# Optimization experiments

Hardware: AMD Instinct MI355X
Metric: run time of the kernel (lower is better)

Reference implementation:

```python
import jax, jax.numpy as jnp
import numpy as np

N = 128          # n_nodes (hardcoded groups=128 in the torch module)
TIME_DIM = 16
XYZ_DIM = 63
SIGMA = 0.3
EPS = 0.01
relu = jax.nn.relu


def gconv(x, W, b):
    # grouped 1x1 Conv1d with groups=N: per-node GEMM
    # x: (N, Cin, L), W: (N, Cout, Cin), b: (N, Cout) -> (N, Cout, L)
    return jnp.einsum('ncl,nkc->nkl', x, W) + b[:, :, None]


def setup_inputs() -> dict:
    key = jax.random.key(0)
    ks = iter(jax.random.split(key, 64))

    def W(shape, fan_in):
        return jax.random.normal(next(ks), shape, jnp.float32) / np.float32(np.sqrt(fan_in))

    def bvec(shape):
        return 0.01 * jax.random.normal(next(ks), shape, jnp.float32)

    B, V = 1, 2048
    inp = {
        'poses': 0.1 * jax.random.normal(next(ks), (B, N, 24, 3), jnp.float32),
        't_ped': jax.random.normal(next(ks), (B, TIME_DIM), jnp.float32),
        'w': jax.random.uniform(next(ks), (N, 24), jnp.float32),
        'wpts': jax.random.uniform(next(ks), (B, V, 3), jnp.float32),
        'nodes_posed': jax.random.uniform(next(ks), (B, N, 3), jnp.float32),
        'local_coords': jax.random.normal(next(ks), (N, B, V, XYZ_DIM), jnp.float32),
        # encoder grouped convs
        'Wec1': W((N, 64, 72 + TIME_DIM), 72 + TIME_DIM), 'bec1': bvec((N, 64)),
        'Wec21': W((N, 8, 64), 64), 'bec21': bvec((N, 8)),
        'Wec22': W((N, 8, 64), 64), 'bec22': bvec((N, 8)),
        # decoder grouped convs
        'Wdc1': W((N, 64, 80), 80), 'bdc1': bvec((N, 64)),
        'Wdc21': W((N, 32, 64), 64), 'bdc21': bvec((N, 32)),
        'Wdc22': W((N, 3, 64), 64), 'bdc22': bvec((N, 3)),
        # feature-field grouped convs
        'Wf1': W((N, 64, 32 + XYZ_DIM), 32 + XYZ_DIM), 'bf1': bvec((N, 64)),
        'Wf2': W((N, 64, 64), 64), 'bf2': bvec((N, 64)),
        'Wf3': W((N, 64, 64), 64), 'bf3': bvec((N, 64)),
        'Wf4': W((N, 256, 64), 64), 'bf4': bvec((N, 256)),
        # Nerf head linears
        'Wc1': W((256, 64), 256), 'bc1': bvec((64,)),
        'Wc2': W((64, 3), 64), 'bc2': bvec((3,)),
        'Wd1': W((256, 1), 256), 'bd1': bvec((1,)),
    }
    return inp


def reference(poses, t_ped, w, wpts, nodes_posed, local_coords,
              Wec1, bec1, Wec21, bec21, Wec22, bec22,
              Wdc1, bdc1, Wdc21, bdc21, Wdc22, bdc22,
              Wf1, bf1, Wf2, bf2, Wf3, bf3, Wf4, bf4,
              Wc1, bc1, Wc2, bc2, Wd1, bd1):
    B, V = poses.shape[0], wpts.shape[1]

    # attention-weighted poses: (B, N, 72)
    poses_w = (w[None, :, :, None] * poses).reshape(B, N, 72)

    # ---- encode ----
    t = jnp.broadcast_to(t_ped[:, None, :], (B, N, TIME_DIM))
    enc_in = jnp.concatenate([poses_w, t], axis=-1).transpose(1, 2, 0)   # (N, 72+td, B)
    net = relu(gconv(enc_in, Wec1, bec1))                                # (N, 64, B)
    mean = gconv(net, Wec21, bec21).transpose(0, 2, 1)                   # (N, B, 8)
    logvar = gconv(net, Wec22, bec22).transpose(0, 2, 1)                 # (N, B, 8)
    z = mean  # eval-mode reparameterize

    # ---- decode ----
    dec_in = jnp.concatenate([poses_w, z.transpose(1, 0, 2)], axis=-1).transpose(1, 2, 0)  # (N, 80, B)
    net = relu(gconv(dec_in, Wdc1, bdc1))
    ei = gconv(net, Wdc21, bdc21).transpose(0, 2, 1)                     # (N, B, 32)
    delta_ni = gconv(net, Wdc22, bdc22).transpose(0, 2, 1)               # (N, B, 3)

    # ---- blend weights: RBF influence of each node on each point ----
    diff = wpts[None, :, :, :] - nodes_posed.transpose(1, 0, 2)[:, :, None, :]  # (N, B, V, 3)
    d2 = jnp.sum(diff * diff, axis=-1)                                   # (N, B, V)
    influ = jnp.exp(-d2 / (2.0 * SIGMA * SIGMA)) - EPS
    mask = influ >= 0
    bweights = jnp.maximum(influ, 0.0)

    # ---- feature field (dense per-node MLP, masked; == padded gather/scatter) ----
    raw = jnp.concatenate([jnp.broadcast_to(ei[:, :, None, :], (N, B, V, 32)),
                           local_coords], axis=-1)                       # (N, B, V, 32+xyz)
    x = raw.reshape(N, B * V, 32 + XYZ_DIM).transpose(0, 2, 1)           # (N, Cin, B*V)
    net = relu(gconv(x, Wf1, bf1))
    net = relu(gconv(net, Wf2, bf2))
    net = relu(gconv(net, Wf3, bf3))
    fout = relu(gconv(net, Wf4, bf4))                                    # (N, 256, B*V)
    f = fout.transpose(0, 2, 1).reshape(N, B, V, 256) * mask[..., None].astype(fout.dtype)

    # ---- blend features ----
    bw = bweights.transpose(1, 2, 0) + 1e-7                              # (B, V, N)
    bw = bw / jnp.sum(bw, axis=-1, keepdims=True)
    f_blend = jnp.einsum('nbvc,bvn->bvc', f, bw)                         # (B, V, 256)

    # ---- Nerf head ----
    netc = relu(f_blend @ Wc1 + bc1)
    c = netc @ Wc2 + bc2                                                 # (B, V, 3)
    d = relu(f_blend @ Wd1 + bd1)                                        # (B, V, 1)
    return (c, d, ei, delta_ni, mean, logvar)
```

## Files before the change

### kernel.cpp

```cpp
#include <hip/hip_runtime.h>

typedef __bf16 bf16;
typedef __bf16 bf16x4 __attribute__((ext_vector_type(4)));
typedef float  f32x4  __attribute__((ext_vector_type(4)));
typedef unsigned short u16x4 __attribute__((ext_vector_type(4)));

#define NPTS 2048
#define LD 68

__global__ __launch_bounds__(256) void k_sniff(const void* poses_raw, int* flag)
{
    __shared__ int cnt;
    if (threadIdx.x == 0) cnt = 0;
    __syncthreads();
    const bf16* pb = (const bf16*)poses_raw;
    int local = 0;
    for (int i = threadIdx.x; i < 9216; i += 256) {
        float v = (float)pb[i];
        if (!(v >= -2.0f && v <= 2.0f)) local++;
    }
    atomicAdd(&cnt, local);
    __syncthreads();
    if (threadIdx.x == 0) *flag = (cnt < 64) ? 1 : 0;
}

template<typename T, int WANT>
__global__ __launch_bounds__(128) void k_encdec_t(
    const T* __restrict__ poses, const T* __restrict__ t_ped, const T* __restrict__ w,
    const T* __restrict__ Wec1, const T* __restrict__ bec1,
    const T* __restrict__ Wec21, const T* __restrict__ bec21,
    const T* __restrict__ Wec22, const T* __restrict__ bec22,
    const T* __restrict__ Wdc1, const T* __restrict__ bdc1,
    const T* __restrict__ Wdc21, const T* __restrict__ bdc21,
    const T* __restrict__ Wdc22, const T* __restrict__ bdc22,
    T* __restrict__ out_ei, T* __restrict__ out_delta,
    T* __restrict__ out_mean, T* __restrict__ out_logvar,
    const int* __restrict__ flag)
{
    if (*flag != WANT) return;
    int n = blockIdx.x, tid = threadIdx.x;
    __shared__ float sin_[88], zbuf[8], net1[64], din[80], net2[64];
    if (tid < 72)      sin_[tid] = (float)w[n*24 + tid/3] * (float)poses[n*72 + tid];
    else if (tid < 88) sin_[tid] = (float)t_ped[tid - 72];
    __syncthreads();
    if (tid < 64) {
        float a = (float)bec1[n*64 + tid];
        const T* wr = Wec1 + (size_t)(n*64 + tid) * 88;
        for (int c = 0; c < 88; ++c) a += (float)wr[c] * sin_[c];
        net1[tid] = fmaxf(a, 0.f);
    }
    __syncthreads();
    if (tid < 8) {
        float a = (float)bec21[n*8 + tid];
        const T* wr = Wec21 + (size_t)(n*8 + tid) * 64;
        for (int c = 0; c < 64; ++c) a += (float)wr[c] * net1[c];
        out_mean[n*8 + tid] = (T)a;
        zbuf[tid] = a;
    } else if (tid < 16) {
        int o = tid - 8;
        float a = (float)bec22[n*8 + o];
        const T* wr = Wec22 + (size_t)(n*8 + o) * 64;
        for (int c = 0; c < 64; ++c) a += (float)wr[c] * net1[c];
        out_logvar[n*8 + o] = (T)a;
    }
    __syncthreads();
    if (tid < 72)      din[tid] = sin_[tid];
    else if (tid < 80) din[tid] = zbuf[tid - 72];
    __syncthreads();
    if (tid < 64) {
        float a = (float)bdc1[n*64 + tid];
        const T* wr = Wdc1 + (size_t)(n*64 + tid) * 80;
        for (int c = 0; c < 80; ++c) a += (float)wr[c] * din[c];
        net2[tid] = fmaxf(a, 0.f);
    }
    __syncthreads();
    if (tid < 32) {
        float a = (float)bdc21[n*32 + tid];
        const T* wr = Wdc21 + (size_t)(n*32 + tid) * 64;
        for (int c = 0; c < 64; ++c) a += (float)wr[c] * net2[c];
        out_ei[n*32 + tid] = (T)a;
    } else if (tid < 35) {
        int o = tid - 32;
        float a = (float)bdc22[n*3 + o];
        const T* wr = Wdc22 + (size_t)(n*3 + o) * 64;
        for (int c = 0; c < 64; ++c) a += (float)wr[c] * net2[c];
        out_delta[n*3 + o] = (T)a;
    }
}

template<typename T, int WANT>
__global__ __launch_bounds__(256) void k_bweights_t(
    const T* __restrict__ wpts, const T* __restrict__ nodes,
    float* __restrict__ wgt, const int* __restrict__ flag)
{
    if (*flag != WANT) return;
    int v = blockIdx.x * 256 + threadIdx.x;
    float px = (float)wpts[v*3+0], py = (float)wpts[v*3+1], pz = (float)wpts[v*3+2];
    float denom = 0.f;
    for (int n = 0; n < 128; ++n) {
        float dx = px - (float)nodes[n*3+0];
        float dy = py - (float)nodes[n*3+1];
        float dz = pz - (float)nodes[n*3+2];
        float d2 = dx*dx + dy*dy + dz*dz;
        float influ = expf(-d2 * (1.0f/0.18f)) - 0.01f;
        denom += fmaxf(influ, 0.f) + 1e-7f;
    }
    float inv = 1.f / denom;
    for (int n = 0; n < 128; ++n) {
        float dx = px - (float)nodes[n*3+0];
        float dy = py - (float)nodes[n*3+1];
        float dz = pz - (float)nodes[n*3+2];
        float d2 = dx*dx + dy*dy + dz*dz;
        float influ = expf(-d2 * (1.0f/0.18f)) - 0.01f;
        wgt[n*NPTS + v] = (influ >= 0.f) ? (fmaxf(influ, 0.f) + 1e-7f) * inv : 0.f;
    }
}

__device__ __forceinline__ f32x4 ld4(const float* p) { return *(const f32x4*)p; }
__device__ __forceinline__ f32x4 ld4(const bf16* p)
{
    bf16x4 v = *(const bf16x4*)p;
    f32x4 r;
    #pragma unroll
    for (int j = 0; j < 4; ++j) r[j] = (float)v[j];
    return r;
}
__device__ __forceinline__ f32x4 ld4_nt(const float* p)
{
    return __builtin_nontemporal_load((const f32x4*)p);
}
__device__ __forceinline__ f32x4 ld4_nt(const bf16* p)
{
    u16x4 u = __builtin_nontemporal_load((const u16x4*)p);
    f32x4 r;
    #pragma unroll
    for (int j = 0; j < 4; ++j) {
        unsigned int bits = ((unsigned int)u[j]) << 16;
        r[j] = __uint_as_float(bits);
    }
    return r;
}

template<typename T, int WANT>
__global__ __launch_bounds__(256) void k_w1prep(
    const T* __restrict__ Wf1, float* __restrict__ W1p, const int* __restrict__ flag)
{
    if (*flag != WANT) return;
    int n = blockIdx.x, tid = threadIdx.x;
    for (int e = tid; e < 6144; e += 256) {
        int oc = e / 96, k = e - oc*96;
        float v = (k < 95) ? (float)Wf1[(size_t)n*6080 + oc*95 + k] : 0.f;
        W1p[(size_t)n*6144 + e] = v;
    }
}

template<typename T>
__device__ __forceinline__ void layer64g(
    const T* __restrict__ W, const T* __restrict__ b,
    const float* __restrict__ hin, float* __restrict__ hout, int og, int pg)
{
    f32x4 acc[4] = {};
    #pragma unroll 4
    for (int k0 = 0; k0 < 64; k0 += 4) {
        f32x4 wv[4], xv[4];
        #pragma unroll
        for (int c = 0; c < 4; ++c) wv[c] = ld4(W + (size_t)(og*4 + c)*64 + k0);
        #pragma unroll
        for (int j = 0; j < 4; ++j) xv[j] = *(const f32x4*)&hin[(k0 + j)*LD + pg*4];
        #pragma unroll
        for (int c = 0; c < 4; ++c)
            #pragma unroll
            for (int j = 0; j < 4; ++j)
                acc[c] += xv[j] * wv[c][j];
    }
    #pragma unroll
    for (int c = 0; c < 4; ++c) {
        float bb = (float)b[og*4 + c];
        f32x4 hv;
        #pragma unroll
        for (int r = 0; r < 4; ++r) hv[r] = fmaxf(acc[c][r] + bb, 0.f);
        *(f32x4*)&hout[(og*4 + c)*LD + pg*4] = hv;
    }
}

template<typename T, int WANT, int W1P>
__global__ __launch_bounds__(256, 3) void k_feat_fast(
    const T* __restrict__ Wf1, const T* __restrict__ Wf2,
    const T* __restrict__ Wf3, const T* __restrict__ Wf4,
    const T* __restrict__ lc, const T* __restrict__ ei,
    const T* __restrict__ bf1, const T* __restrict__ bf2,
    const T* __restrict__ bf3, const T* __restrict__ bf4,
    const float* __restrict__ wgt, const float* __restrict__ W1p,
    int nslice, float* __restrict__ slices, float* __restrict__ f_blend,
    const int* __restrict__ flag)
{
    if (*flag != WANT) return;
    int bid = blockIdx.x;
    int xcd = bid & 7;
    int i   = bid >> 3;
    int g     = 2*xcd + (i >> 5);
    int ptile = i & 31;
    int p0  = ptile * 64;
    int tid = threadIdx.x;
    int og = tid >> 4;
    int pg = tid & 15;

    __shared__ __attribute__((aligned(16))) float smem[(96 + 64) * LD];
    float* xs = smem;
    float* hA = smem + 96*LD;

    if (tid < 64) xs[95*LD + tid] = 0.f;

    f32x4 fb[4][4];
    #pragma unroll
    for (int a = 0; a < 4; ++a)
        #pragma unroll
        for (int c = 0; c < 4; ++c) fb[a][c] = (f32x4){0.f,0.f,0.f,0.f};

    f32x4 lv[4];

    auto stage_load = [&](int n) {
        const T* src = lc + ((size_t)n*NPTS + p0) * 63;
        if (tid < 252) {
            #pragma unroll
            for (int j = 0; j < 4; ++j) lv[j] = ld4_nt(src + tid*16 + j*4);
        }
    };
    auto stage_write = [&](int n) {
        if (tid < 252) {
            #pragma unroll
            for (int j = 0; j < 4; ++j)
                #pragma unroll
                for (int l = 0; l < 4; ++l) {
                    int e = tid*16 + j*4 + l;
                    int p = e/63, c = e - 63*p;
                    xs[(32 + c)*LD + p] = lv[j][l];
                }
        }
        const T* ein = ei + n*32;
        #pragma unroll
        for (int k = 0; k < 8; ++k) {
            int e = k*256 + tid;
            int row = e >> 6, p = e & 63;
            xs[row*LD + p] = (float)ein[row];
        }
    };

    stage_load(g*8);
    stage_write(g*8);
    __syncthreads();

    #pragma unroll 1
    for (int nn = 0; nn < 8; ++nn) {
        int n = g*8 + nn;

        if (W1P) {
            const float* W1b = W1p + (size_t)(n*64 + og*4) * 96;
            f32x4 acc[4] = {};
            #pragma unroll 4
            for (int k0 = 0; k0 < 96; k0 += 4) {
                f32x4 wv[4], xv[4];
                #pragma unroll
                for (int c = 0; c < 4; ++c) wv[c] = ld4(W1b + (size_t)c*96 + k0);
                #pragma unroll
                for (int j = 0; j < 4; ++j) xv[j] = *(const f32x4*)&xs[(k0 + j)*LD + pg*4];
                #pragma unroll
                for (int c = 0; c < 4; ++c)
                    #pragma unroll
                    for (int j = 0; j < 4; ++j)
                        acc[c] += xv[j] * wv[c][j];
            }
            #pragma unroll
            for (int c = 0; c < 4; ++c) {
                float bb = (float)bf1[n*64 + og*4 + c];
                f32x4 hv;
                #pragma unroll
                for (int r = 0; r < 4; ++r) hv[r] = fmaxf(acc[c][r] + bb, 0.f);
                *(f32x4*)&hA[(og*4 + c)*LD + pg*4] = hv;
            }
        } else {
            const T* W1b = Wf1 + (size_t)(n*64 + og*4) * 95;
            f32x4 acc[4] = {};
            #pragma unroll 4
            for (int kk = 0; kk < 23; ++kk) {
                int k0 = kk*4;
                float wv[4][4]; f32x4 xv[4];
                #pragma unroll
                for (int c = 0; c < 4; ++c) {
                    const T* wr = W1b + (size_t)c*95 + k0;
                    #pragma unroll
                    for (int j = 0; j < 4; ++j) wv[c][j] = (float)wr[j];
                }
                #pragma unroll
                for (int j = 0; j < 4; ++j) xv[j] = *(const f32x4*)&xs[(k0 + j)*LD + pg*4];
                #pragma unroll
                for (int c = 0; c < 4; ++c)
                    #pragma unroll
                    for (int j = 0; j < 4; ++j)
                        acc[c] += xv[j] * wv[c][j];
            }
            {
                f32x4 xt[3];
                #pragma unroll
                for (int j = 0; j < 3; ++j) xt[j] = *(const f32x4*)&xs[(92 + j)*LD + pg*4];
                #pragma unroll
                for (int c = 0; c < 4; ++c) {
                    const T* wr = W1b + (size_t)c*95;
                    #pragma unroll
                    for (int j = 0; j < 3; ++j)
                        acc[c] += xt[j] * (float)wr[92 + j];
                }
            }
            #pragma unroll
            for (int c = 0; c < 4; ++c) {
                float bb = (float)bf1[n*64 + og*4 + c];
                f32x4 hv;
                #pragma unroll
                for (int r = 0; r < 4; ++r) hv[r] = fmaxf(acc[c][r] + bb, 0.f);
                *(f32x4*)&hA[(og*4 + c)*LD + pg*4] = hv;
            }
        }
        __syncthreads();

        layer64g(Wf2 + (size_t)n*64*64, bf2 + n*64, hA, xs, og, pg);
        __syncthreads();

        layer64g(Wf3 + (size_t)n*64*64, bf3 + n*64, xs, hA, og, pg);
        __syncthreads();

        if (nn < 7) stage_load(n + 1);

        {
            f32x4 wgtv = ld4_nt(wgt + (size_t)n*NPTS + p0 + pg*4);
            const T* W4n = Wf4 + (size_t)n*256*64;
            const T* b4n = bf4 + n*256;
            #pragma unroll 1
            for (int mt = 0; mt < 4; ++mt) {
                f32x4 acc[4] = {};
                #pragma unroll 4
                for (int k0 = 0; k0 < 64; k0 += 4) {
                    f32x4 wv[4], xv[4];
                    #pragma unroll
                    for (int c = 0; c < 4; ++c)
                        wv[c] = ld4(W4n + (size_t)(mt*64 + og*4 + c)*64 + k0);
                    #pragma unroll
                    for (int j = 0; j < 4; ++j) xv[j] = *(const f32x4*)&hA[(k0 + j)*LD + pg*4];
                    #pragma unroll
                    for (int c = 0; c < 4; ++c)
                        #pragma unroll
                        for (int j = 0; j < 4; ++j)
                            acc[c] += xv[j] * wv[c][j];
                }
                #pragma unroll
                for (int c = 0; c < 4; ++c) {
                    float bb = (float)b4n[mt*64 + og*4 + c];
                    #pragma unroll
                    for (int r = 0; r < 4; ++r)
                        fb[mt][c][r] += fmaxf(acc[c][r] + bb, 0.f) * wgtv[r];
                }
            }
        }
        if (nn < 7) stage_write(n + 1);
        __syncthreads();
    }

    bool atom = (g >= nslice);
    float* dst = atom ? f_blend : (slices + (size_t)g*NPTS*256);
    float* tbuf = smem;
    #pragma unroll 1
    for (int qq = 0; qq < 4; ++qq) {
        if (qq) __syncthreads();
        if ((pg >> 2) == qq) {
            #pragma unroll
            for (int mt = 0; mt < 4; ++mt)
                #pragma unroll
                for (int r = 0; r < 4; ++r) {
                    int row = (pg & 3)*4 + r;
                    f32x4 v = { fb[mt][0][r], fb[mt][1][r], fb[mt][2][r], fb[mt][3][r] };
                    *(f32x4*)&tbuf[row*260 + mt*64 + og*4] = v;
                }
        }
        __syncthreads();
        #pragma unroll
        for (int k = 0; k < 4; ++k) {
            int idx = k*1024 + tid*4;
            int row = idx >> 8, col = idx & 255;
            f32x4 v = *(const f32x4*)&tbuf[row*260 + col];
            size_t o = ((size_t)(p0 + qq*16 + row))*256 + col;
            if (atom) {
                #pragma unroll
                for (int j = 0; j < 4; ++j) atomicAdd(&f_blend[o + j], v[j]);
            } else {
                __builtin_nontemporal_store(v, (f32x4*)&dst[o]);
            }
        }
    }
}

template<int WANT>
__global__ __launch_bounds__(256) void k_reduce(
    const float* __restrict__ slices, float* __restrict__ fbl,
    int nslice, const int* __restrict__ flag)
{
    if (*flag != WANT) return;
    size_t t = (size_t)(blockIdx.x*256 + threadIdx.x) * 4;
    f32x4 s = *(const f32x4*)&fbl[t];
    for (int gg = 0; gg < nslice; ++gg)
        s += __builtin_nontemporal_load((const f32x4*)&slices[(size_t)gg*NPTS*256 + t]);
    *(f32x4*)&fbl[t] = s;
}

__global__ __launch_bounds__(256) void k_zero_fb(float* __restrict__ fb)
{
    fb[blockIdx.x*256 + threadIdx.x] = 0.f;
}

template<typename T, int WANT>
__global__ __launch_bounds__(256) void k_head_t(
    const float* __restrict__ f_blend,
    const T* __restrict__ Wc1, const T* __restrict__ bc1,
    const T* __restrict__ Wc2, const T* __restrict__ bc2,
    const T* __restrict__ Wd1, const T* __restrict__ bd1,
    T* __restrict__ out_c, T* __restrict__ out_d,
    const int* __restrict__ flag)
{
    if (*flag != WANT) return;
    int t = blockIdx.x * 256 + threadIdx.x;
    int p = t >> 6, j = t & 63;
    const float* fb = f_blend + (size_t)p * 256;

    float a = (float)bc1[j];
    #pragma unroll 8
    for (int c = 0; c < 256; ++c)
        a += fb[c] * (float)Wc1[c*64 + j];
    float nc = fmaxf(a, 0.f);

    float s0 = nc * (float)Wc2[j*3 + 0];
    float s1 = nc * (float)Wc2[j*3 + 1];
    float s2 = nc * (float)Wc2[j*3 + 2];
    float sd = 0.f;
    #pragma unroll
    for (int u = 0; u < 4; ++u) {
        int c = j*4 + u;
        sd += fb[c] * (float)Wd1[c];
    }
    #pragma unroll
    for (int off = 32; off > 0; off >>= 1) {
        s0 += __shfl_down(s0, off);
        s1 += __shfl_down(s1, off);
        s2 += __shfl_down(s2, off);
        sd += __shfl_down(sd, off);
    }
    if (j == 0) {
        out_c[p*3 + 0] = (T)(s0 + (float)bc2[0]);
        out_c[p*3 + 1] = (T)(s1 + (float)bc2[1]);
        out_c[p*3 + 2] = (T)(s2 + (float)bc2[2]);
        out_d[p]       = (T)fmaxf(sd + (float)bd1[0], 0.f);
    }
}

extern "C" void kernel_launch(void* const* d_in, const int* in_sizes, int n_in,
                              void* d_out, int out_size, void* d_ws, size_t ws_size,
                              hipStream_t stream)
{
    const size_t SLICE_BYTES = (size_t)NPTS * 256 * 4;
    const size_t W1P_BYTES   = (size_t)128 * 64 * 96 * 4;

    char* wsp = (char*)d_ws;
    auto alloc = [&](size_t bytes) { char* r = wsp; wsp += (bytes + 255) & ~(size_t)255; return r; };
    float* f_blend = (float*)alloc(SLICE_BYTES);
    float* wgt     = (float*)alloc((size_t)128 * NPTS * 4);
    int*   flag    = (int*)  alloc(256);

    float* W1p = nullptr;
    bool use_w1p = ((size_t)(wsp - (char*)d_ws) + W1P_BYTES) <= ws_size;
    if (use_w1p) W1p = (float*)alloc(W1P_BYTES);

    int nslice = 0;
    float* slices = (float*)wsp;
    while (nslice < 16 && ((size_t)(wsp - (char*)d_ws) + SLICE_BYTES) <= ws_size) {
        alloc(SLICE_BYTES);
        nslice++;
    }

    hipLaunchKernelGGL(k_sniff, dim3(1), dim3(256), 0, stream, d_in[0], flag);
    hipLaunchKernelGGL(k_zero_fb, dim3(2048), dim3(256), 0, stream, f_blend);

    #define LAUNCH_ALL(T, WANT)                                                         \
    {                                                                                   \
        const T* poses = (const T*)d_in[0];                                             \
        const T* t_ped = (const T*)d_in[1];                                             \
        const T* w     = (const T*)d_in[2];                                             \
        const T* wpts  = (const T*)d_in[3];                                             \
        const T* nodes = (const T*)d_in[4];                                             \
        const T* lc    = (const T*)d_in[5];                                             \
        const T* Wec1  = (const T*)d_in[6];  const T* bec1 = (const T*)d_in[7];         \
        const T* Wec21 = (const T*)d_in[8];  const T* bec21= (const T*)d_in[9];         \
        const T* Wec22 = (const T*)d_in[10]; const T* bec22= (const T*)d_in[11];        \
        const T* Wdc1  = (const T*)d_in[12]; const T* bdc1 = (const T*)d_in[13];        \
        const T* Wdc21 = (const T*)d_in[14]; const T* bdc21= (const T*)d_in[15];        \
        const T* Wdc22 = (const T*)d_in[16]; const T* bdc22= (const T*)d_in[17];        \
        const T* Wf1   = (const T*)d_in[18]; const T* bf1  = (const T*)d_in[19];        \
        const T* Wf2   = (const T*)d_in[20]; const T* bf2  = (const T*)d_in[21];        \
        const T* Wf3   = (const T*)d_in[22]; const T* bf3  = (const T*)d_in[23];        \
        const T* Wf4   = (const T*)d_in[24]; const T* bf4  = (const T*)d_in[25];        \
        const T* Wc1   = (const T*)d_in[26]; const T* bc1  = (const T*)d_in[27];        \
        const T* Wc2   = (const T*)d_in[28]; const T* bc2  = (const T*)d_in[29];        \
        const T* Wd1   = (const T*)d_in[30]; const T* bd1  = (const T*)d_in[31];        \
        T* out = (T*)d_out;                                                             \
        T* out_c      = out;                                                            \
        T* out_d      = out + 6144;                                                     \
        T* out_ei     = out + 8192;                                                     \
        T* out_delta  = out + 12288;                                                    \
        T* out_mean   = out + 12672;                                                    \
        T* out_logvar = out + 13696;                                                    \
        hipLaunchKernelGGL((k_encdec_t<T, WANT>), dim3(128), dim3(128), 0, stream,      \
            poses, t_ped, w, Wec1, bec1, Wec21, bec21, Wec22, bec22,                    \
            Wdc1, bdc1, Wdc21, bdc21, Wdc22, bdc22,                                     \
            out_ei, out_delta, out_mean, out_logvar, flag);                             \
        hipLaunchKernelGGL((k_bweights_t<T, WANT>), dim3(8), dim3(256), 0, stream,      \
            wpts, nodes, wgt, flag);                                                    \
        if (use_w1p)                                                                    \
            hipLaunchKernelGGL((k_w1prep<T, WANT>), dim3(128), dim3(256), 0, stream,    \
                Wf1, W1p, flag);                                                        \
        if (use_w1p)                                                                    \
            hipLaunchKernelGGL((k_feat_fast<T, WANT, 1>), dim3(512), dim3(256), 0,      \
                stream, Wf1, Wf2, Wf3, Wf4, lc, (const T*)out_ei,                       \
                bf1, bf2, bf3, bf4, wgt, W1p, nslice, slices, f_blend, flag);           \
        else                                                                            \
            hipLaunchKernelGGL((k_feat_fast<T, WANT, 0>), dim3(512), dim3(256), 0,      \
                stream, Wf1, Wf2, Wf3, Wf4, lc, (const T*)out_ei,                       \
                bf1, bf2, bf3, bf4, wgt, W1p, nslice, slices, f_blend, flag);           \
        if (nslice > 0)                                                                 \
            hipLaunchKernelGGL((k_reduce<WANT>), dim3(512), dim3(256), 0, stream,       \
                slices, f_blend, nslice, flag);                                         \
        hipLaunchKernelGGL((k_head_t<T, WANT>), dim3(512), dim3(256), 0, stream,        \
            f_blend, Wc1, bc1, Wc2, bc2, Wd1, bd1, out_c, out_d, flag);                 \
    }

    LAUNCH_ALL(bf16, 1)
    LAUNCH_ALL(float, 0)
    #undef LAUNCH_ALL
}
```

Before: 603.3 us.

## Compute feature layers in place in one LDS buffer, double grid, atomics into per-XCD slices

Removes the second LDS activation buffer by running layers 2 and 3 in place, with extra barriers between the reads and the writes. The smaller LDS footprint allows 4 blocks per CU. Each block now processes 4 nodes instead of 8, so the grid doubles to 1024 blocks. The final writes become atomic adds into per-XCD partial slices (zeroed up front) that are then reduced, or straight into f_blend when there is no workspace. This trades extra barriers, a larger zeroing pass and more atomic traffic for higher occupancy and parallelism.

New measurement: 788.2 us. +30.6%, slower.

```diff
diff --git a/kernel.cpp b/kernel.cpp
--- a/kernel.cpp
+++ b/kernel.cpp
@@ -155,9 +155,9 @@
 }
 
 template<typename T>
-__device__ __forceinline__ void layer64g(
+__device__ __forceinline__ void layer64_ip(
     const T* __restrict__ W, const T* __restrict__ b,
-    const float* __restrict__ hin, float* __restrict__ hout, int og, int pg)
+    float* __restrict__ xs, int og, int pg)
 {
     f32x4 acc[4] = {};
     #pragma unroll 4
@@ -166,48 +166,48 @@
         #pragma unroll
         for (int c = 0; c < 4; ++c) wv[c] = ld4(W + (size_t)(og*4 + c)*64 + k0);
         #pragma unroll
-        for (int j = 0; j < 4; ++j) xv[j] = *(const f32x4*)&hin[(k0 + j)*LD + pg*4];
+        for (int j = 0; j < 4; ++j) xv[j] = *(const f32x4*)&xs[(k0 + j)*LD + pg*4];
         #pragma unroll
         for (int c = 0; c < 4; ++c)
             #pragma unroll
             for (int j = 0; j < 4; ++j)
                 acc[c] += xv[j] * wv[c][j];
     }
+    __syncthreads();
     #pragma unroll
     for (int c = 0; c < 4; ++c) {
         float bb = (float)b[og*4 + c];
         f32x4 hv;
         #pragma unroll
         for (int r = 0; r < 4; ++r) hv[r] = fmaxf(acc[c][r] + bb, 0.f);
-        *(f32x4*)&hout[(og*4 + c)*LD + pg*4] = hv;
-    }
+        *(f32x4*)&xs[(og*4 + c)*LD + pg*4] = hv;
+    }
+    __syncthreads();
 }
 
 template<typename T, int WANT, int W1P>
-__global__ __launch_bounds__(256, 3) void k_feat_fast(
+__global__ __launch_bounds__(256, 4) void k_feat_fast(
     const T* __restrict__ Wf1, const T* __restrict__ Wf2,
     const T* __restrict__ Wf3, const T* __restrict__ Wf4,
     const T* __restrict__ lc, const T* __restrict__ ei,
     const T* __restrict__ bf1, const T* __restrict__ bf2,
     const T* __restrict__ bf3, const T* __restrict__ bf4,
     const float* __restrict__ wgt, const float* __restrict__ W1p,
-    int nslice, float* __restrict__ slices, float* __restrict__ f_blend,
+    int shift, float* __restrict__ slices,
     const int* __restrict__ flag)
 {
     if (*flag != WANT) return;
     int bid = blockIdx.x;
     int xcd = bid & 7;
     int i   = bid >> 3;
-    int g     = 2*xcd + (i >> 5);
+    int g     = 4*xcd + (i >> 5);
     int ptile = i & 31;
     int p0  = ptile * 64;
     int tid = threadIdx.x;
     int og = tid >> 4;
     int pg = tid & 15;
 
-    __shared__ __attribute__((aligned(16))) float smem[(96 + 64) * LD];
-    float* xs = smem;
-    float* hA = smem + 96*LD;
+    __shared__ __attribute__((aligned(16))) float xs[96 * LD];
 
     if (tid < 64) xs[95*LD + tid] = 0.f;
 
@@ -246,89 +246,80 @@
         }
     };
 
-    stage_load(g*8);
-    stage_write(g*8);
+    stage_load(g*4);
+    stage_write(g*4);
     __syncthreads();
 
     #pragma unroll 1
-    for (int nn = 0; nn < 8; ++nn) {
-        int n = g*8 + nn;
-
-        if (W1P) {
-            const float* W1b = W1p + (size_t)(n*64 + og*4) * 96;
+    for (int nn = 0; nn < 4; ++nn) {
+        int n = g*4 + nn;
+
+        {
             f32x4 acc[4] = {};
-            #pragma unroll 4
-            for (int k0 = 0; k0 < 96; k0 += 4) {
-                f32x4 wv[4], xv[4];
-                #pragma unroll
-                for (int c = 0; c < 4; ++c) wv[c] = ld4(W1b + (size_t)c*96 + k0);
-                #pragma unroll
-                for (int j = 0; j < 4; ++j) xv[j] = *(const f32x4*)&xs[(k0 + j)*LD + pg*4];
-                #pragma unroll
-                for (int c = 0; c < 4; ++c)
-                    #pragma unroll
-                    for (int j = 0; j < 4; ++j)
-                        acc[c] += xv[j] * wv[c][j];
+            if (W1P) {
+                const float* W1b = W1p + (size_t)(n*64 + og*4) * 96;
+                #pragma unroll 4
+                for (int k0 = 0; k0 < 96; k0 += 4) {
+                    f32x4 wv[4], xv[4];
+                    #pragma unroll
+                    for (int c = 0; c < 4; ++c) wv[c] = ld4(W1b + (size_t)c*96 + k0);
+                    #pragma unroll
+                    for (int j = 0; j < 4; ++j) xv[j] = *(const f32x4*)&xs[(k0 + j)*LD + pg*4];
+                    #pragma unroll
+                    for (int c = 0; c < 4; ++c)
+                        #pragma unroll
+                        for (int j = 0; j < 4; ++j)
+                            acc[c] += xv[j] * wv[c][j];
+                }
+            } else {
+                const T* W1b = Wf1 + (size_t)(n*64 + og*4) * 95;
+                #pragma unroll 4
+                for (int kk = 0; kk < 23; ++kk) {
+                    int k0 = kk*4;
+                    float wv[4][4]; f32x4 xv[4];
+                    #pragma unroll
+                    for (int c = 0; c < 4; ++c) {
+                        const T* wr = W1b + (size_t)c*95 + k0;
+                        #pragma unroll
+                        for (int j = 0; j < 4; ++j) wv[c][j] = (float)wr[j];
+                    }
+                    #pragma unroll
+                    for (int j = 0; j < 4; ++j) xv[j] = *(const f32x4*)&xs[(k0 + j)*LD + pg*4];
+                    #pragma unroll
+                    for (int c = 0; c < 4; ++c)
+                        #pragma unroll
+                        for (int j = 0; j < 4; ++j)
+                            acc[c] += xv[j] * wv[c][j];
+                }
+                {
+                    f32x4 xt[3];
+                    #pragma unroll
+                    for (int j = 0; j < 3; ++j) xt[j] = *(const f32x4*)&xs[(92 + j)*LD + pg*4];
+                    #pragma unroll
+                    for (int c = 0; c < 4; ++c) {
+                        const T* wr = W1b + (size_t)c*95;
+                        #pragma unroll
+                        for (int j = 0; j < 3; ++j)
+                            acc[c] += xt[j] * (float)wr[92 + j];
+                    }
+                }
             }
+            __syncthreads();
             #pragma unroll
             for (int c = 0; c < 4; ++c) {
                 float bb = (float)bf1[n*64 + og*4 + c];
                 f32x4 hv;
                 #pragma unroll
                 for (int r = 0; r < 4; ++r) hv[r] = fmaxf(acc[c][r] + bb, 0.f);
-                *(f32x4*)&hA[(og*4 + c)*LD + pg*4] = hv;
+                *(f32x4*)&xs[(og*4 + c)*LD + pg*4] = hv;
             }
-        } else {
-            const T* W1b = Wf1 + (size_t)(n*64 + og*4) * 95;
-            f32x4 acc[4] = {};
-            #pragma unroll 4
-            for (int kk = 0; kk < 23; ++kk) {
-                int k0 = kk*4;
-                float wv[4][4]; f32x4 xv[4];
-                #pragma unroll
-                for (int c = 0; c < 4; ++c) {
-                    const T* wr = W1b + (size_t)c*95 + k0;
-                    #pragma unroll
-                    for (int j = 0; j < 4; ++j) wv[c][j] = (float)wr[j];
-                }
-                #pragma unroll
-                for (int j = 0; j < 4; ++j) xv[j] = *(const f32x4*)&xs[(k0 + j)*LD + pg*4];
-                #pragma unroll
-                for (int c = 0; c < 4; ++c)
-                    #pragma unroll
-                    for (int j = 0; j < 4; ++j)
-                        acc[c] += xv[j] * wv[c][j];
-            }
-            {
-                f32x4 xt[3];
-                #pragma unroll
-                for (int j = 0; j < 3; ++j) xt[j] = *(const f32x4*)&xs[(92 + j)*LD + pg*4];
-                #pragma unroll
-                for (int c = 0; c < 4; ++c) {
-                    const T* wr = W1b + (size_t)c*95;
-                    #pragma unroll
-                    for (int j = 0; j < 3; ++j)
-                        acc[c] += xt[j] * (float)wr[92 + j];
-                }
-            }
-            #pragma unroll
-            for (int c = 0; c < 4; ++c) {
-                float bb = (float)bf1[n*64 + og*4 + c];
-                f32x4 hv;
-                #pragma unroll
-                for (int r = 0; r < 4; ++r) hv[r] = fmaxf(acc[c][r] + bb, 0.f);
-                *(f32x4*)&hA[(og*4 + c)*LD + pg*4] = hv;
-            }
-        }
-        __syncthreads();
-
-        layer64g(Wf2 + (size_t)n*64*64, bf2 + n*64, hA, xs, og, pg);
-        __syncthreads();
-
-        layer64g(Wf3 + (size_t)n*64*64, bf3 + n*64, xs, hA, og, pg);
-        __syncthreads();
-
-        if (nn < 7) stage_load(n + 1);
+            __syncthreads();
+        }
+
+        layer64_ip(Wf2 + (size_t)n*64*64, bf2 + n*64, xs, og, pg);
+        layer64_ip(Wf3 + (size_t)n*64*64, bf3 + n*64, xs, og, pg);
+
+        if (nn < 3) stage_load(n + 1);
 
         {
             f32x4 wgtv = ld4_nt(wgt + (size_t)n*NPTS + p0 + pg*4);
@@ -344,7 +335,7 @@
                     for (int c = 0; c < 4; ++c)
                         wv[c] = ld4(W4n + (size_t)(mt*64 + og*4 + c)*64 + k0);
                     #pragma unroll
-                    for (int j = 0; j < 4; ++j) xv[j] = *(const f32x4*)&hA[(k0 + j)*LD + pg*4];
+                    for (int j = 0; j < 4; ++j) xv[j] = *(const f32x4*)&xs[(k0 + j)*LD + pg*4];
                     #pragma unroll
                     for (int c = 0; c < 4; ++c)
                         #pragma unroll
@@ -360,13 +351,12 @@
                 }
             }
         }
-        if (nn < 7) stage_write(n + 1);
         __syncthreads();
-    }
-
-    bool atom = (g >= nslice);
-    float* dst = atom ? f_blend : (slices + (size_t)g*NPTS*256);
-    float* tbuf = smem;
+        if (nn < 3) { stage_write(n + 1); __syncthreads(); }
+    }
+
+    float* dst = slices + (size_t)(xcd >> shift) * NPTS * 256;
+    float* tbuf = xs;
     #pragma unroll 1
     for (int qq = 0; qq < 4; ++qq) {
         if (qq) __syncthreads();
@@ -387,12 +377,8 @@
             int row = idx >> 8, col = idx & 255;
             f32x4 v = *(const f32x4*)&tbuf[row*260 + col];
             size_t o = ((size_t)(p0 + qq*16 + row))*256 + col;
-            if (atom) {
-                #pragma unroll
-                for (int j = 0; j < 4; ++j) atomicAdd(&f_blend[o + j], v[j]);
-            } else {
-                __builtin_nontemporal_store(v, (f32x4*)&dst[o]);
-            }
+            #pragma unroll
+            for (int j = 0; j < 4; ++j) atomicAdd(&dst[o + j], v[j]);
         }
     }
 }
@@ -404,7 +390,7 @@
 {
     if (*flag != WANT) return;
     size_t t = (size_t)(blockIdx.x*256 + threadIdx.x) * 4;
-    f32x4 s = *(const f32x4*)&fbl[t];
+    f32x4 s = {};
     for (int gg = 0; gg < nslice; ++gg)
         s += __builtin_nontemporal_load((const f32x4*)&slices[(size_t)gg*NPTS*256 + t]);
     *(f32x4*)&fbl[t] = s;
@@ -412,7 +398,7 @@
 
 __global__ __launch_bounds__(256) void k_zero_fb(float* __restrict__ fb)
 {
-    fb[blockIdx.x*256 + threadIdx.x] = 0.f;
+    fb[(size_t)blockIdx.x*256 + threadIdx.x] = 0.f;
 }
 
 template<typename T, int WANT>
@@ -477,14 +463,20 @@
     if (use_w1p) W1p = (float*)alloc(W1P_BYTES);
 
     int nslice = 0;
-    float* slices = (float*)wsp;
-    while (nslice < 16 && ((size_t)(wsp - (char*)d_ws) + SLICE_BYTES) <= ws_size) {
-        alloc(SLICE_BYTES);
-        nslice++;
-    }
+    float* slices = nullptr;
+    for (int cand = 8; cand >= 1; cand >>= 1) {
+        if ((size_t)(wsp - (char*)d_ws) + (size_t)cand*SLICE_BYTES <= ws_size) {
+            slices = (float*)alloc((size_t)cand*SLICE_BYTES);
+            nslice = cand;
+            break;
+        }
+    }
+    bool skip_reduce = false;
+    if (nslice == 0) { slices = f_blend; nslice = 1; skip_reduce = true; }
+    int shift = (nslice == 8) ? 0 : (nslice == 4) ? 1 : (nslice == 2) ? 2 : 3;
 
     hipLaunchKernelGGL(k_sniff, dim3(1), dim3(256), 0, stream, d_in[0], flag);
-    hipLaunchKernelGGL(k_zero_fb, dim3(2048), dim3(256), 0, stream, f_blend);
+    hipLaunchKernelGGL(k_zero_fb, dim3(nslice * 2048), dim3(256), 0, stream, slices);
 
     #define LAUNCH_ALL(T, WANT)                                                         \
     {                                                                                   \
@@ -520,18 +512,18 @@
             out_ei, out_delta, out_mean, out_logvar, flag);                             \
         hipLaunchKernelGGL((k_bweights_t<T, WANT>), dim3(8), dim3(256), 0, stream,      \
             wpts, nodes, wgt, flag);                                                    \
-        if (use_w1p)                                                                    \
+        if (use_w1p) {                                                                  \
             hipLaunchKernelGGL((k_w1prep<T, WANT>), dim3(128), dim3(256), 0, stream,    \
                 Wf1, W1p, flag);                                                        \
-        if (use_w1p)                                                                    \
-            hipLaunchKernelGGL((k_feat_fast<T, WANT, 1>), dim3(512), dim3(256), 0,      \
+            hipLaunchKernelGGL((k_feat_fast<T, WANT, 1>), dim3(1024), dim3(256), 0,     \
                 stream, Wf1, Wf2, Wf3, Wf4, lc, (const T*)out_ei,                       \
-                bf1, bf2, bf3, bf4, wgt, W1p, nslice, slices, f_blend, flag);           \
-        else                                                                            \
-            hipLaunchKernelGGL((k_feat_fast<T, WANT, 0>), dim3(512), dim3(256), 0,      \
+                bf1, bf2, bf3, bf4, wgt, W1p, shift, slices, flag);                     \
+        } else {                                                                        \
+            hipLaunchKernelGGL((k_feat_fast<T, WANT, 0>), dim3(1024), dim3(256), 0,     \
                 stream, Wf1, Wf2, Wf3, Wf4, lc, (const T*)out_ei,                       \
-                bf1, bf2, bf3, bf4, wgt, W1p, nslice, slices, f_blend, flag);           \
-        if (nslice > 0)                                                                 \
+                bf1, bf2, bf3, bf4, wgt, W1p, shift, slices, flag);                     \
+        }                                                                               \
+        if (!skip_reduce)                                                               \
             hipLaunchKernelGGL((k_reduce<WANT>), dim3(512), dim3(256), 0, stream,       \
                 slices, f_blend, nslice, flag);                                         \
         hipLaunchKernelGGL((k_head_t<T, WANT>), dim3(512), dim3(256), 0, stream,        \
```
